# Kernel optimization log

Hardware: AMD Instinct MI355X
Metric: run time of the kernel (lower is better)

The kernel has to match this reference:

```python
import jax, jax.numpy as jnp
import numpy as np

B, S, C = 4, 4096, 1024
H, D, K = 16, 64, 256  # nhead, head_dim, dim_k


def setup_inputs() -> dict:
    key = jax.random.key(0)
    ks = jax.random.split(key, 7)
    x = jax.random.normal(ks[0], (B, S, C), dtype=jnp.float32)
    # per-head QKV projection weights (torch Linear weight layout [out,in])
    Wq = jax.random.normal(ks[1], (H, D, C), dtype=jnp.float32) * (C ** -0.5)
    Wk = jax.random.normal(ks[2], (H, D, C), dtype=jnp.float32) * (C ** -0.5)
    Wv = jax.random.normal(ks[3], (H, D, C), dtype=jnp.float32) * (C ** -0.5)
    # Linformer E/F sequence projections, per head: [K, S]
    We = jax.random.normal(ks[4], (H, K, S), dtype=jnp.float32) * (S ** -0.5)
    Wf = jax.random.normal(ks[5], (H, K, S), dtype=jnp.float32) * (S ** -0.5)
    # output projection (with bias, as w_o is nn.Linear default bias=True)
    Wo = jax.random.normal(ks[6], (C, H * D), dtype=jnp.float32) * ((H * D) ** -0.5)
    bo = jnp.zeros((C,), dtype=jnp.float32)
    return {"x": x, "Wq": Wq, "Wk": Wk, "Wv": Wv, "We": We, "Wf": Wf, "Wo": Wo, "bo": bo}


def reference(x, Wq, Wk, Wv, We, Wf, Wo, bo):
    # per-head projections: [B,H,S,D]
    Q = jnp.einsum('bsc,hdc->bhsd', x, Wq)
    Kh = jnp.einsum('bsc,hdc->bhsd', x, Wk)
    Vh = jnp.einsum('bsc,hdc->bhsd', x, Wv)
    # E-projection of K over the sequence axis: K^T [B,H,D,S] -> [B,H,D,K]
    Kp = jnp.einsum('bhsd,hks->bhdk', Kh, We)
    # scores: Q @ E(K^T) / sqrt(head_dim), softmax over low-rank axis k
    scale = 1.0 / jnp.sqrt(jnp.asarray(D, dtype=x.dtype))
    P = jax.nn.softmax(jnp.einsum('bhsd,bhdk->bhsk', Q, Kp) * scale, axis=-1)
    # F-projection of V over the sequence axis, then transpose back: [B,H,K,D]
    Vp = jnp.einsum('bhsd,hks->bhkd', Vh, Wf)
    out = jnp.einsum('bhsk,bhkd->bhsd', P, Vp)          # [B,H,S,D]
    out = out.transpose(0, 2, 1, 3).reshape(B, S, H * D)  # concat heads
    return jnp.einsum('bse,ce->bsc', out, Wo) + bo       # w_o (dropout=0)
```

## Files before the change

### kernel.cpp

```cpp
#include <hip/hip_runtime.h>
#include <stdint.h>


typedef unsigned short u16;
typedef __bf16 bf16t;
typedef bf16t bf16x8 __attribute__((ext_vector_type(8)));
typedef float f32x4 __attribute__((ext_vector_type(4)));

#define MFMA16(a, b, c) __builtin_amdgcn_mfma_f32_16x16x32_bf16((a), (b), (c), 0, 0, 0)

__device__ __forceinline__ u16 f2bf(float f) {
  return __builtin_bit_cast(u16, (bf16t)f);
}

__device__ __forceinline__ bf16x8 ldf(const u16* p) { return *(const bf16x8*)p; }

__device__ __forceinline__ void gload16(const void* g, void* l) {
  __builtin_amdgcn_global_load_lds(
      (__attribute__((address_space(1))) void*)g,
      (__attribute__((address_space(3))) void*)l, 16, 0, 0);
}

__device__ __forceinline__ int xcd_swz(int orig, int nwg) {
  return (orig & 7) * (nwg >> 3) + (orig >> 3);
}

__global__ __launch_bounds__(256) void cvt_all(
    const float* __restrict__ x, const float* __restrict__ We,
    const float* __restrict__ Wf, const float* __restrict__ Wq,
    const float* __restrict__ Wk, const float* __restrict__ Wv,
    const float* __restrict__ Wo, u16* __restrict__ xb, u16* __restrict__ web,
    u16* __restrict__ wfb, u16* __restrict__ wqkv, u16* __restrict__ wob) {
  const int stride = gridDim.x * 256;
  for (int i = blockIdx.x * 256 + threadIdx.x; i < 13631488; i += stride) {
    const float4* s;
    ushort4* d;
    int off;
    if (i < 8388608) {
      if (i < 4194304) { s = (const float4*)x;  d = (ushort4*)xb;  off = i; }
      else             { s = (const float4*)We; d = (ushort4*)web; off = i - 4194304; }
    } else if (i < 12582912) { s = (const float4*)Wf; d = (ushort4*)wfb; off = i - 8388608; }
    else if (i < 12845056)   { s = (const float4*)Wq; d = (ushort4*)wqkv; off = i - 12582912; }
    else if (i < 13107200)   { s = (const float4*)Wk; d = (ushort4*)wqkv + 262144; off = i - 12845056; }
    else if (i < 13369344)   { s = (const float4*)Wv; d = (ushort4*)wqkv + 524288; off = i - 13107200; }
    else                     { s = (const float4*)Wo; d = (ushort4*)wob; off = i - 13369344; }
    float4 v = s[off];
    ushort4 o;
    o.x = f2bf(v.x); o.y = f2bf(v.y); o.z = f2bf(v.z); o.w = f2bf(v.w);
    d[off] = o;
  }
}

__global__ __launch_bounds__(256) void gemm_q(const u16* __restrict__ A,
                                              const u16* __restrict__ BT,
                                              u16* __restrict__ Qd) {
  __shared__ u16 As[128 * 32];
  __shared__ u16 Bs[128 * 32];
  const int wg = xcd_swz(blockIdx.x, 1024);
  const int m0 = (wg >> 3) * 128, n0 = (wg & 7) * 128;
  const int tid = threadIdx.x, w = tid >> 6, l = tid & 63, g = l >> 4, r = l & 15;
  const int wm = (w >> 1) * 64, wn = (w & 1) * 64;
  const u16* Ab = A + (size_t)m0 * 1024;
  const u16* Bb = BT + (size_t)n0 * 1024;
  f32x4 acc[4][4] = {};
  for (int kt = 0; kt < 32; ++kt) {
    const int k0 = kt * 32;
    __syncthreads();
#pragma unroll
    for (int i = 0; i < 2; ++i) {
      const int c = i * 256 + w * 64 + l;
      const int row = c >> 2, co = (c & 3) * 8;
      gload16(Ab + (size_t)row * 1024 + k0 + co, As + (i * 256 + w * 64) * 8);
      gload16(Bb + (size_t)row * 1024 + k0 + co, Bs + (i * 256 + w * 64) * 8);
    }
    __syncthreads();
    bf16x8 af[4], bfv[4];
#pragma unroll
    for (int fm = 0; fm < 4; ++fm) af[fm] = ldf(As + (wm + fm * 16 + r) * 32 + g * 8);
#pragma unroll
    for (int fn = 0; fn < 4; ++fn) bfv[fn] = ldf(Bs + (wn + fn * 16 + r) * 32 + g * 8);
#pragma unroll
    for (int fm = 0; fm < 4; ++fm)
#pragma unroll
      for (int fn = 0; fn < 4; ++fn)
        acc[fm][fn] = MFMA16(af[fm], bfv[fn], acc[fm][fn]);
  }
#pragma unroll
  for (int fm = 0; fm < 4; ++fm)
#pragma unroll
    for (int fn = 0; fn < 4; ++fn)
#pragma unroll
      for (int j = 0; j < 4; ++j) {
        const int m = m0 + wm + fm * 16 + g * 4 + j;
        const int n = n0 + wn + fn * 16 + r;
        const int b = m >> 12, s = m & 4095, h = n >> 6, d = n & 63;
        Qd[(((size_t)(b * 16 + h)) * 4096 + s) * 64 + d] = f2bf(acc[fm][fn][j] * 0.125f);
      }
}

__global__ __launch_bounds__(256) void gemm_kv(const u16* __restrict__ A,
                                               const u16* __restrict__ BT,
                                               u16* __restrict__ KTd,
                                               u16* __restrict__ VTd) {
  __shared__ u16 As[128 * 32];
  __shared__ u16 Bs[128 * 32];
  const int wg = xcd_swz(blockIdx.x, 2048);
  const int m0 = (wg & 15) * 128, n0 = (wg >> 4) * 128;
  const int tid = threadIdx.x, w = tid >> 6, l = tid & 63, g = l >> 4, r = l & 15;
  const int wm = (w >> 1) * 64, wn = (w & 1) * 64;
  const u16* Ab = A + (size_t)m0 * 1024;
  const u16* Bb = BT + (size_t)n0 * 1024;
  f32x4 acc[4][4] = {};
  for (int kt = 0; kt < 32; ++kt) {
    const int k0 = kt * 32;
    __syncthreads();
#pragma unroll
    for (int i = 0; i < 2; ++i) {
      const int c = i * 256 + w * 64 + l;
      const int row = c >> 2, co = (c & 3) * 8;
      gload16(Ab + (size_t)row * 1024 + k0 + co, As + (i * 256 + w * 64) * 8);
      gload16(Bb + (size_t)row * 1024 + k0 + co, Bs + (i * 256 + w * 64) * 8);
    }
    __syncthreads();
    bf16x8 af[4], bfv[4];
#pragma unroll
    for (int fm = 0; fm < 4; ++fm) af[fm] = ldf(As + (wm + fm * 16 + r) * 32 + g * 8);
#pragma unroll
    for (int fn = 0; fn < 4; ++fn) bfv[fn] = ldf(Bs + (wn + fn * 16 + r) * 32 + g * 8);
#pragma unroll
    for (int fm = 0; fm < 4; ++fm)
#pragma unroll
      for (int fn = 0; fn < 4; ++fn)
        acc[fm][fn] = MFMA16(af[fm], bfv[fn], acc[fm][fn]);
  }
#pragma unroll
  for (int fm = 0; fm < 4; ++fm)
#pragma unroll
    for (int fn = 0; fn < 4; ++fn)
#pragma unroll
      for (int j = 0; j < 4; ++j) {
        const int m = m0 + wm + fm * 16 + g * 4 + j;
        const int n = n0 + wn + fn * 16 + r;
        const int which = m >> 10, hd = m & 1023, h = hd >> 6, d = hd & 63;
        const int b = n >> 12, s = n & 4095;
        u16* dst = which ? VTd : KTd;
        dst[(((size_t)(b * 16 + h)) * 64 + d) * 4096 + s] = f2bf(acc[fm][fn][j]);
      }
}

__global__ __launch_bounds__(256) void gemm_small(const u16* __restrict__ web,
                                                  const u16* __restrict__ wfb,
                                                  const u16* __restrict__ KT,
                                                  const u16* __restrict__ VT,
                                                  float* __restrict__ part) {
  __shared__ u16 ldsBig[256 * 64];
  __shared__ u16 ldsSml[64 * 64];
  const int bx = blockIdx.x, chunk = blockIdx.y;
  const int mode = bx & 1;
  const int bh = bx >> 1;
  const int hh = bh & 15;
  const u16 *Ap, *Bp;
  int M, N;
  u16 *ldsA, *ldsB;
  if (mode == 0) {
    Ap = web + (size_t)hh * 256 * 4096;
    Bp = KT + (size_t)bh * 64 * 4096;
    M = 256; N = 64;
    ldsA = ldsBig; ldsB = ldsSml;
  } else {
    Ap = VT + (size_t)bh * 64 * 4096;
    Bp = wfb + (size_t)hh * 256 * 4096;
    M = 64; N = 256;
    ldsA = ldsSml; ldsB = ldsBig;
  }
  float* Cpf = part + ((size_t)(mode * 4 + chunk) * 64 + bh) * 16384;
  const int tid = threadIdx.x, w = tid >> 6, l = tid & 63, g = l >> 4, r = l & 15;
  const int mb = (mode == 0) ? w * 64 : 0;
  const int nb = (mode == 0) ? 0 : w * 64;
  const int iA = (M * 8) / 256, iB = (N * 8) / 256;
  f32x4 acc[4][4] = {};
  for (int kt = chunk * 16; kt < chunk * 16 + 16; ++kt) {
    const int k0 = kt * 64;
    __syncthreads();
    for (int i = 0; i < iA; ++i) {
      const int c = w * (M * 2) + i * 64 + l;
      const int row = c >> 3, co = (c & 7) * 8;
      gload16(Ap + (size_t)row * 4096 + k0 + co, ldsA + (w * (M * 2) + i * 64) * 8);
    }
    for (int i = 0; i < iB; ++i) {
      const int c = w * (N * 2) + i * 64 + l;
      const int row = c >> 3, co = (c & 7) * 8;
      gload16(Bp + (size_t)row * 4096 + k0 + co, ldsB + (w * (N * 2) + i * 64) * 8);
    }
    __syncthreads();
#pragma unroll
    for (int kk = 0; kk < 2; ++kk) {
      bf16x8 af[4], bfv[4];
#pragma unroll
      for (int fm = 0; fm < 4; ++fm)
        af[fm] = ldf(ldsA + (mb + fm * 16 + r) * 64 + kk * 32 + g * 8);
#pragma unroll
      for (int fn = 0; fn < 4; ++fn)
        bfv[fn] = ldf(ldsB + (nb + fn * 16 + r) * 64 + kk * 32 + g * 8);
#pragma unroll
      for (int fm = 0; fm < 4; ++fm)
#pragma unroll
        for (int fn = 0; fn < 4; ++fn)
          acc[fm][fn] = MFMA16(af[fm], bfv[fn], acc[fm][fn]);
    }
  }
#pragma unroll
  for (int fm = 0; fm < 4; ++fm)
#pragma unroll
    for (int fn = 0; fn < 4; ++fn)
#pragma unroll
      for (int j = 0; j < 4; ++j) {
        const int m = mb + fm * 16 + g * 4 + j;
        const int n = nb + fn * 16 + r;
        Cpf[(size_t)m * N + n] = acc[fm][fn][j];
      }
}

__global__ __launch_bounds__(256) void reduce_small(const float* __restrict__ part,
                                                    u16* __restrict__ Kp,
                                                    u16* __restrict__ VpT) {
  const int i4 = blockIdx.x * 256 + threadIdx.x;
  const int mode = i4 >> 18;
  const int r4 = i4 & 262143;
  const float4* b = (const float4*)part;
  float4 s0 = b[(size_t)(mode * 4 + 0) * 262144 + r4];
  float4 s1 = b[(size_t)(mode * 4 + 1) * 262144 + r4];
  float4 s2 = b[(size_t)(mode * 4 + 2) * 262144 + r4];
  float4 s3 = b[(size_t)(mode * 4 + 3) * 262144 + r4];
  ushort4 o;
  o.x = f2bf(s0.x + s1.x + s2.x + s3.x);
  o.y = f2bf(s0.y + s1.y + s2.y + s3.y);
  o.z = f2bf(s0.z + s1.z + s2.z + s3.z);
  o.w = f2bf(s0.w + s1.w + s2.w + s3.w);
  ushort4* dst = (ushort4*)(mode ? VpT : Kp);
  dst[r4] = o;
}

__global__ __launch_bounds__(256, 1) void attn_fused(const u16* __restrict__ Q,
                                                     const u16* __restrict__ Kp,
                                                     const u16* __restrict__ VpT,
                                                     u16* __restrict__ att) {
  __shared__ u16 P[4][16 * 264];
  const int gid = blockIdx.x;
  const int bh = gid >> 3;
  const int st = gid & 7;
  const int hh = bh & 15, b = bh >> 4;
  const int tid = threadIdx.x, w = tid >> 6, l = tid & 63, g = l >> 4, r = l & 15;
  const u16* Kpb = Kp + (size_t)bh * 256 * 64;
  const u16* Vb = VpT + (size_t)bh * 64 * 256;

  bf16x8 kf[32];
  bf16x8 vf[32];
#pragma unroll
  for (int fn = 0; fn < 16; ++fn) {
    kf[fn * 2 + 0] = ldf(Kpb + (fn * 16 + r) * 64 + g * 8);
    kf[fn * 2 + 1] = ldf(Kpb + (fn * 16 + r) * 64 + 32 + g * 8);
  }
#pragma unroll
  for (int fn2 = 0; fn2 < 4; ++fn2)
#pragma unroll
    for (int kk = 0; kk < 8; ++kk)
      vf[fn2 * 8 + kk] = ldf(Vb + (fn2 * 16 + r) * 256 + kk * 32 + g * 8);

  u16* Pw = P[w];
  for (int t = 0; t < 8; ++t) {
    const int s0 = st * 512 + t * 64 + w * 16;
    const u16* Qb = Q + ((size_t)bh * 4096 + s0) * 64;
    const bf16x8 qf0 = ldf(Qb + r * 64 + g * 8);
    const bf16x8 qf1 = ldf(Qb + r * 64 + 32 + g * 8);
    f32x4 sc[16];
#pragma unroll
    for (int fn = 0; fn < 16; ++fn) {
      sc[fn] = MFMA16(qf0, kf[fn * 2 + 0], (f32x4){});
      sc[fn] = MFMA16(qf1, kf[fn * 2 + 1], sc[fn]);
    }
    float rinv[4];
#pragma unroll
    for (int j = 0; j < 4; ++j) {
      float sum = 0.f;
#pragma unroll
      for (int fn = 0; fn < 16; ++fn) {
        const float e = __expf(sc[fn][j]);
        sc[fn][j] = e;
        sum += e;
      }
      sum += __shfl_xor(sum, 1);
      sum += __shfl_xor(sum, 2);
      sum += __shfl_xor(sum, 4);
      sum += __shfl_xor(sum, 8);
      rinv[j] = 1.0f / sum;
    }
#pragma unroll
    for (int fn = 0; fn < 16; ++fn)
#pragma unroll
      for (int j = 0; j < 4; ++j)
        Pw[(g * 4 + j) * 264 + fn * 16 + r] = f2bf(sc[fn][j]);

    f32x4 o[4] = {};
#pragma unroll
    for (int kk = 0; kk < 8; ++kk) {
      const bf16x8 pa = ldf(Pw + r * 264 + kk * 32 + g * 8);
#pragma unroll
      for (int fn2 = 0; fn2 < 4; ++fn2)
        o[fn2] = MFMA16(pa, vf[fn2 * 8 + kk], o[fn2]);
    }
#pragma unroll
    for (int fn2 = 0; fn2 < 4; ++fn2)
#pragma unroll
      for (int j = 0; j < 4; ++j) {
        const int s = s0 + g * 4 + j;
        const int d = fn2 * 16 + r;
        att[((size_t)b * 4096 + s) * 1024 + hh * 64 + d] = f2bf(o[fn2][j] * rinv[j]);
      }
  }
}

__global__ __launch_bounds__(256) void gemm_out(const u16* __restrict__ A,
                                                const u16* __restrict__ BT,
                                                const float* __restrict__ bo,
                                                float* __restrict__ out) {
  __shared__ u16 As[128 * 32];
  __shared__ u16 Bs[128 * 32];
  const int wg = xcd_swz(blockIdx.x, 1024);
  const int m0 = (wg >> 3) * 128, n0 = (wg & 7) * 128;
  const int tid = threadIdx.x, w = tid >> 6, l = tid & 63, g = l >> 4, r = l & 15;
  const int wm = (w >> 1) * 64, wn = (w & 1) * 64;
  const u16* Ab = A + (size_t)m0 * 1024;
  const u16* Bb = BT + (size_t)n0 * 1024;
  f32x4 acc[4][4] = {};
  for (int kt = 0; kt < 32; ++kt) {
    const int k0 = kt * 32;
    __syncthreads();
#pragma unroll
    for (int i = 0; i < 2; ++i) {
      const int c = i * 256 + w * 64 + l;
      const int row = c >> 2, co = (c & 3) * 8;
      gload16(Ab + (size_t)row * 1024 + k0 + co, As + (i * 256 + w * 64) * 8);
      gload16(Bb + (size_t)row * 1024 + k0 + co, Bs + (i * 256 + w * 64) * 8);
    }
    __syncthreads();
    bf16x8 af[4], bfv[4];
#pragma unroll
    for (int fm = 0; fm < 4; ++fm) af[fm] = ldf(As + (wm + fm * 16 + r) * 32 + g * 8);
#pragma unroll
    for (int fn = 0; fn < 4; ++fn) bfv[fn] = ldf(Bs + (wn + fn * 16 + r) * 32 + g * 8);
#pragma unroll
    for (int fm = 0; fm < 4; ++fm)
#pragma unroll
      for (int fn = 0; fn < 4; ++fn)
        acc[fm][fn] = MFMA16(af[fm], bfv[fn], acc[fm][fn]);
  }
#pragma unroll
  for (int fm = 0; fm < 4; ++fm)
#pragma unroll
    for (int fn = 0; fn < 4; ++fn)
#pragma unroll
      for (int j = 0; j < 4; ++j) {
        const int m = m0 + wm + fm * 16 + g * 4 + j;
        const int n = n0 + wn + fn * 16 + r;
        out[(size_t)m * 1024 + n] = acc[fm][fn][j] + bo[n];
      }
}

extern "C" void kernel_launch(void* const* d_in, const int* in_sizes, int n_in,
                              void* d_out, int out_size, void* d_ws, size_t ws_size,
                              hipStream_t stream) {
  (void)in_sizes; (void)n_in; (void)out_size; (void)ws_size;
  const float* x  = (const float*)d_in[0];
  const float* Wq = (const float*)d_in[1];
  const float* Wk = (const float*)d_in[2];
  const float* Wv = (const float*)d_in[3];
  const float* We = (const float*)d_in[4];
  const float* Wf = (const float*)d_in[5];
  const float* Wo = (const float*)d_in[6];
  const float* bo = (const float*)d_in[7];
  char* ws = (char*)d_ws;
  u16* xb    = (u16*)(ws + 0);
  float* prt = (float*)(ws + 0);
  u16* att   = (u16*)(ws + 0);
  u16* wqkv  = (u16*)(ws + 33554432);
  u16* web   = (u16*)(ws + 39845888);
  u16* wfb   = (u16*)(ws + 73400320);
  u16* wob   = (u16*)(ws + 106954752);
  u16* Qd    = (u16*)(ws + 109051904);
  u16* KTd   = (u16*)(ws + 142606336);
  u16* VTd   = (u16*)(ws + 176160768);
  u16* Kpd   = (u16*)(ws + 209715200);
  u16* VpTd  = (u16*)(ws + 211812352);

  cvt_all<<<2048, 256, 0, stream>>>(x, We, Wf, Wq, Wk, Wv, Wo, xb, web, wfb, wqkv, wob);
  gemm_q<<<1024, 256, 0, stream>>>(xb, wqkv, Qd);
  gemm_kv<<<2048, 256, 0, stream>>>(wqkv + 1048576, xb, KTd, VTd);
  gemm_small<<<dim3(128, 4), 256, 0, stream>>>(web, wfb, KTd, VTd, prt);
  reduce_small<<<2048, 256, 0, stream>>>(prt, Kpd, VpTd);
  attn_fused<<<512, 256, 0, stream>>>(Qd, Kpd, VpTd, att);
  gemm_out<<<1024, 256, 0, stream>>>(att, wob, bo, (float*)d_out);
}
```

Measured before the change: 356.1 us.

## Rewrite projection GEMMs as 256x256 double-buffered LDS-swizzled tiles with 512 threads

Replaces the three 128x128, single-buffered, BK=32 GEMM kernels (Q, KV, output projection) with a shared 256x256 tile mainloop using 8 waves, BK=64, double-buffered global-to-LDS loads with partial vmcnt waits, and an XOR-swizzled LDS layout to avoid bank conflicts. MFMA sections are raised in priority with s_setprio. This is meant to raise arithmetic intensity per tile and overlap loads with compute. The cost is 128KB of LDS per block and larger accumulator register use, which could limit occupancy, and with fewer blocks there may be tail-effect risk.

```diff
diff --git a/kernel.cpp b/kernel.cpp
--- a/kernel.cpp
+++ b/kernel.cpp
@@ -23,6 +23,65 @@
 
 __device__ __forceinline__ int xcd_swz(int orig, int nwg) {
   return (orig & 7) * (nwg >> 3) + (orig >> 3);
+}
+
+__device__ __forceinline__ void gemm256_main(const u16* __restrict__ A,
+                                             const u16* __restrict__ BT,
+                                             int m0, int n0, f32x4 acc[8][4],
+                                             u16* sm) {
+  const int tid = threadIdx.x;
+  const int w = tid >> 6, l = tid & 63, g = l >> 4, r = l & 15;
+  const int wr = w >> 2, wc = w & 3;
+  const int rowt = tid >> 3;
+  const int cbsw = ((tid & 7) * 16) ^ ((rowt & 7) << 4);
+  const int sxor = (r & 7) << 4;
+  const char* Ab = (const char*)A;
+  const char* Bb = (const char*)BT;
+  char* smc = (char*)sm;
+
+  auto stage = [&](int T, int buf) {
+    const int k0 = T * 64;
+#pragma unroll
+    for (int i = 0; i < 4; ++i) {
+      const int row = i * 64 + rowt;
+      gload16(Ab + (((size_t)(m0 + row) << 10) + k0) * 2 + cbsw,
+              smc + buf * 32768 + i * 8192 + w * 1024);
+      gload16(Bb + (((size_t)(n0 + row) << 10) + k0) * 2 + cbsw,
+              smc + 65536 + buf * 32768 + i * 8192 + w * 1024);
+    }
+  };
+
+  stage(0, 0);
+  for (int t = 0; t < 16; ++t) {
+    const int b = t & 1;
+    stage(t < 15 ? t + 1 : 15, b ^ 1);
+    asm volatile("s_waitcnt vmcnt(8)" ::: "memory");
+    __builtin_amdgcn_s_barrier();
+    asm volatile("" ::: "memory");
+    const char* At = smc + b * 32768;
+    const char* Bt = smc + 65536 + b * 32768;
+#pragma unroll
+    for (int kk = 0; kk < 2; ++kk) {
+      const int cb = (kk * 64 + g * 16) ^ sxor;
+      bf16x8 af[8], bf[4];
+#pragma unroll
+      for (int m = 0; m < 8; ++m)
+        af[m] = *(const bf16x8*)(At + ((wr * 128 + m * 16 + r) * 128 + cb));
+#pragma unroll
+      for (int n = 0; n < 4; ++n)
+        bf[n] = *(const bf16x8*)(Bt + ((wc * 64 + n * 16 + r) * 128 + cb));
+      __builtin_amdgcn_s_setprio(1);
+#pragma unroll
+      for (int m = 0; m < 8; ++m)
+#pragma unroll
+        for (int n = 0; n < 4; ++n)
+          acc[m][n] = MFMA16(af[m], bf[n], acc[m][n]);
+      __builtin_amdgcn_s_setprio(0);
+    }
+    asm volatile("" ::: "memory");
+    __builtin_amdgcn_s_barrier();
+    asm volatile("" ::: "memory");
+  }
 }
 
 __global__ __launch_bounds__(256) void cvt_all(
@@ -51,100 +110,75 @@
   }
 }
 
-__global__ __launch_bounds__(256) void gemm_q(const u16* __restrict__ A,
-                                              const u16* __restrict__ BT,
-                                              u16* __restrict__ Qd) {
-  __shared__ u16 As[128 * 32];
-  __shared__ u16 Bs[128 * 32];
-  const int wg = xcd_swz(blockIdx.x, 1024);
-  const int m0 = (wg >> 3) * 128, n0 = (wg & 7) * 128;
-  const int tid = threadIdx.x, w = tid >> 6, l = tid & 63, g = l >> 4, r = l & 15;
-  const int wm = (w >> 1) * 64, wn = (w & 1) * 64;
-  const u16* Ab = A + (size_t)m0 * 1024;
-  const u16* Bb = BT + (size_t)n0 * 1024;
-  f32x4 acc[4][4] = {};
-  for (int kt = 0; kt < 32; ++kt) {
-    const int k0 = kt * 32;
-    __syncthreads();
-#pragma unroll
-    for (int i = 0; i < 2; ++i) {
-      const int c = i * 256 + w * 64 + l;
-      const int row = c >> 2, co = (c & 3) * 8;
-      gload16(Ab + (size_t)row * 1024 + k0 + co, As + (i * 256 + w * 64) * 8);
-      gload16(Bb + (size_t)row * 1024 + k0 + co, Bs + (i * 256 + w * 64) * 8);
-    }
-    __syncthreads();
-    bf16x8 af[4], bfv[4];
-#pragma unroll
-    for (int fm = 0; fm < 4; ++fm) af[fm] = ldf(As + (wm + fm * 16 + r) * 32 + g * 8);
-#pragma unroll
-    for (int fn = 0; fn < 4; ++fn) bfv[fn] = ldf(Bs + (wn + fn * 16 + r) * 32 + g * 8);
-#pragma unroll
-    for (int fm = 0; fm < 4; ++fm)
-#pragma unroll
-      for (int fn = 0; fn < 4; ++fn)
-        acc[fm][fn] = MFMA16(af[fm], bfv[fn], acc[fm][fn]);
-  }
-#pragma unroll
-  for (int fm = 0; fm < 4; ++fm)
-#pragma unroll
-    for (int fn = 0; fn < 4; ++fn)
-#pragma unroll
-      for (int j = 0; j < 4; ++j) {
-        const int m = m0 + wm + fm * 16 + g * 4 + j;
-        const int n = n0 + wn + fn * 16 + r;
-        const int b = m >> 12, s = m & 4095, h = n >> 6, d = n & 63;
-        Qd[(((size_t)(b * 16 + h)) * 4096 + s) * 64 + d] = f2bf(acc[fm][fn][j] * 0.125f);
-      }
-}
-
-__global__ __launch_bounds__(256) void gemm_kv(const u16* __restrict__ A,
-                                               const u16* __restrict__ BT,
-                                               u16* __restrict__ KTd,
-                                               u16* __restrict__ VTd) {
-  __shared__ u16 As[128 * 32];
-  __shared__ u16 Bs[128 * 32];
-  const int wg = xcd_swz(blockIdx.x, 2048);
-  const int m0 = (wg & 15) * 128, n0 = (wg >> 4) * 128;
-  const int tid = threadIdx.x, w = tid >> 6, l = tid & 63, g = l >> 4, r = l & 15;
-  const int wm = (w >> 1) * 64, wn = (w & 1) * 64;
-  const u16* Ab = A + (size_t)m0 * 1024;
-  const u16* Bb = BT + (size_t)n0 * 1024;
-  f32x4 acc[4][4] = {};
-  for (int kt = 0; kt < 32; ++kt) {
-    const int k0 = kt * 32;
-    __syncthreads();
-#pragma unroll
-    for (int i = 0; i < 2; ++i) {
-      const int c = i * 256 + w * 64 + l;
-      const int row = c >> 2, co = (c & 3) * 8;
-      gload16(Ab + (size_t)row * 1024 + k0 + co, As + (i * 256 + w * 64) * 8);
-      gload16(Bb + (size_t)row * 1024 + k0 + co, Bs + (i * 256 + w * 64) * 8);
-    }
-    __syncthreads();
-    bf16x8 af[4], bfv[4];
-#pragma unroll
-    for (int fm = 0; fm < 4; ++fm) af[fm] = ldf(As + (wm + fm * 16 + r) * 32 + g * 8);
-#pragma unroll
-    for (int fn = 0; fn < 4; ++fn) bfv[fn] = ldf(Bs + (wn + fn * 16 + r) * 32 + g * 8);
-#pragma unroll
-    for (int fm = 0; fm < 4; ++fm)
-#pragma unroll
-      for (int fn = 0; fn < 4; ++fn)
-        acc[fm][fn] = MFMA16(af[fm], bfv[fn], acc[fm][fn]);
-  }
-#pragma unroll
-  for (int fm = 0; fm < 4; ++fm)
-#pragma unroll
-    for (int fn = 0; fn < 4; ++fn)
-#pragma unroll
-      for (int j = 0; j < 4; ++j) {
-        const int m = m0 + wm + fm * 16 + g * 4 + j;
-        const int n = n0 + wn + fn * 16 + r;
-        const int which = m >> 10, hd = m & 1023, h = hd >> 6, d = hd & 63;
-        const int b = n >> 12, s = n & 4095;
+__global__ __launch_bounds__(512, 2) void gemm_q(const u16* __restrict__ A,
+                                                 const u16* __restrict__ BT,
+                                                 u16* __restrict__ Qd) {
+  __shared__ u16 sm[65536];
+  const int wg = xcd_swz(blockIdx.x, 256);
+  const int m0 = (wg >> 2) * 256, n0 = (wg & 3) * 256;
+  const int tid = threadIdx.x, w = tid >> 6, l = tid & 63, g = l >> 4, r = l & 15;
+  const int wr = w >> 2, wc = w & 3;
+  f32x4 acc[8][4] = {};
+  gemm256_main(A, BT, m0, n0, acc, sm);
+#pragma unroll
+  for (int m = 0; m < 8; ++m)
+#pragma unroll
+    for (int n = 0; n < 4; ++n)
+#pragma unroll
+      for (int j = 0; j < 4; ++j) {
+        const int mm = m0 + wr * 128 + m * 16 + g * 4 + j;
+        const int nn = n0 + wc * 64 + n * 16 + r;
+        const int b = mm >> 12, s = mm & 4095, h = nn >> 6, d = nn & 63;
+        Qd[(((size_t)(b * 16 + h)) * 4096 + s) * 64 + d] = f2bf(acc[m][n][j] * 0.125f);
+      }
+}
+
+__global__ __launch_bounds__(512, 2) void gemm_kv(const u16* __restrict__ A,
+                                                  const u16* __restrict__ BT,
+                                                  u16* __restrict__ KTd,
+                                                  u16* __restrict__ VTd) {
+  __shared__ u16 sm[65536];
+  const int wg = xcd_swz(blockIdx.x, 512);
+  const int m0 = (wg & 7) * 256, n0 = (wg >> 3) * 256;
+  const int tid = threadIdx.x, w = tid >> 6, l = tid & 63, g = l >> 4, r = l & 15;
+  const int wr = w >> 2, wc = w & 3;
+  f32x4 acc[8][4] = {};
+  gemm256_main(A, BT, m0, n0, acc, sm);
+#pragma unroll
+  for (int m = 0; m < 8; ++m)
+#pragma unroll
+    for (int n = 0; n < 4; ++n)
+#pragma unroll
+      for (int j = 0; j < 4; ++j) {
+        const int mm = m0 + wr * 128 + m * 16 + g * 4 + j;
+        const int nn = n0 + wc * 64 + n * 16 + r;
+        const int which = mm >> 10, hd = mm & 1023, h = hd >> 6, d = hd & 63;
+        const int b = nn >> 12, s = nn & 4095;
         u16* dst = which ? VTd : KTd;
-        dst[(((size_t)(b * 16 + h)) * 64 + d) * 4096 + s] = f2bf(acc[fm][fn][j]);
+        dst[(((size_t)(b * 16 + h)) * 64 + d) * 4096 + s] = f2bf(acc[m][n][j]);
+      }
+}
+
+__global__ __launch_bounds__(512, 2) void gemm_out(const u16* __restrict__ A,
+                                                   const u16* __restrict__ BT,
+                                                   const float* __restrict__ bo,
+                                                   float* __restrict__ out) {
+  __shared__ u16 sm[65536];
+  const int wg = xcd_swz(blockIdx.x, 256);
+  const int m0 = (wg >> 2) * 256, n0 = (wg & 3) * 256;
+  const int tid = threadIdx.x, w = tid >> 6, l = tid & 63, g = l >> 4, r = l & 15;
+  const int wr = w >> 2, wc = w & 3;
+  f32x4 acc[8][4] = {};
+  gemm256_main(A, BT, m0, n0, acc, sm);
+#pragma unroll
+  for (int m = 0; m < 8; ++m)
+#pragma unroll
+    for (int n = 0; n < 4; ++n)
+#pragma unroll
+      for (int j = 0; j < 4; ++j) {
+        const int mm = m0 + wr * 128 + m * 16 + g * 4 + j;
+        const int nn = n0 + wc * 64 + n * 16 + r;
+        out[(size_t)mm * 1024 + nn] = acc[m][n][j] + bo[nn];
       }
 }
 
@@ -318,53 +352,6 @@
         att[((size_t)b * 4096 + s) * 1024 + hh * 64 + d] = f2bf(o[fn2][j] * rinv[j]);
       }
   }
-}
-
-__global__ __launch_bounds__(256) void gemm_out(const u16* __restrict__ A,
-                                                const u16* __restrict__ BT,
-                                                const float* __restrict__ bo,
-                                                float* __restrict__ out) {
-  __shared__ u16 As[128 * 32];
-  __shared__ u16 Bs[128 * 32];
-  const int wg = xcd_swz(blockIdx.x, 1024);
-  const int m0 = (wg >> 3) * 128, n0 = (wg & 7) * 128;
-  const int tid = threadIdx.x, w = tid >> 6, l = tid & 63, g = l >> 4, r = l & 15;
-  const int wm = (w >> 1) * 64, wn = (w & 1) * 64;
-  const u16* Ab = A + (size_t)m0 * 1024;
-  const u16* Bb = BT + (size_t)n0 * 1024;
-  f32x4 acc[4][4] = {};
-  for (int kt = 0; kt < 32; ++kt) {
-    const int k0 = kt * 32;
-    __syncthreads();
-#pragma unroll
-    for (int i = 0; i < 2; ++i) {
-      const int c = i * 256 + w * 64 + l;
-      const int row = c >> 2, co = (c & 3) * 8;
-      gload16(Ab + (size_t)row * 1024 + k0 + co, As + (i * 256 + w * 64) * 8);
-      gload16(Bb + (size_t)row * 1024 + k0 + co, Bs + (i * 256 + w * 64) * 8);
-    }
-    __syncthreads();
-    bf16x8 af[4], bfv[4];
-#pragma unroll
-    for (int fm = 0; fm < 4; ++fm) af[fm] = ldf(As + (wm + fm * 16 + r) * 32 + g * 8);
-#pragma unroll
-    for (int fn = 0; fn < 4; ++fn) bfv[fn] = ldf(Bs + (wn + fn * 16 + r) * 32 + g * 8);
-#pragma unroll
-    for (int fm = 0; fm < 4; ++fm)
-#pragma unroll
-      for (int fn = 0; fn < 4; ++fn)
-        acc[fm][fn] = MFMA16(af[fm], bfv[fn], acc[fm][fn]);
-  }
-#pragma unroll
-  for (int fm = 0; fm < 4; ++fm)
-#pragma unroll
-    for (int fn = 0; fn < 4; ++fn)
-#pragma unroll
-      for (int j = 0; j < 4; ++j) {
-        const int m = m0 + wm + fm * 16 + g * 4 + j;
-        const int n = n0 + wn + fn * 16 + r;
-        out[(size_t)m * 1024 + n] = acc[fm][fn][j] + bo[n];
-      }
 }
 
 extern "C" void kernel_launch(void* const* d_in, const int* in_sizes, int n_in,
@@ -394,10 +381,10 @@
   u16* VpTd  = (u16*)(ws + 211812352);
 
   cvt_all<<<2048, 256, 0, stream>>>(x, We, Wf, Wq, Wk, Wv, Wo, xb, web, wfb, wqkv, wob);
-  gemm_q<<<1024, 256, 0, stream>>>(xb, wqkv, Qd);
-  gemm_kv<<<2048, 256, 0, stream>>>(wqkv + 1048576, xb, KTd, VTd);
+  gemm_q<<<256, 512, 0, stream>>>(xb, wqkv, Qd);
+  gemm_kv<<<512, 512, 0, stream>>>(wqkv + 1048576, xb, KTd, VTd);
   gemm_small<<<dim3(128, 4), 256, 0, stream>>>(web, wfb, KTd, VTd, prt);
   reduce_small<<<2048, 256, 0, stream>>>(prt, Kpd, VpTd);
   attn_fused<<<512, 256, 0, stream>>>(Qd, Kpd, VpTd, att);
-  gemm_out<<<1024, 256, 0, stream>>>(att, wob, bo, (float*)d_out);
-}
+  gemm_out<<<256, 512, 0, stream>>>(att, wob, bo, (float*)d_out);
+}
```

Result: faster. 328.1 us (-7.9%).
